# Kernel optimization log

Measured on AMD Instinct MI355X. Metric: run time of the kernel, lower is better.

Reference implementation:

```python
import jax, jax.numpy as jnp
import numpy as np

B = 2; C = 128; HEADS = 4
D, H, W = 16, 56, 56
WD, WH, WW = 8, 7, 7
SD, SH, SW = 4, 3, 3
N = WD * WH * WW  # 392 tokens per window
ND, NH, NW = D // WD, H // WH, W // WW
NWIN = ND * NH * NW  # windows per batch element
EPS = 1e-5

def _rel_index():
    # standard Swin3D relative position index, [N, N]
    coords = np.stack(np.meshgrid(np.arange(WD), np.arange(WH), np.arange(WW), indexing='ij'))
    coords = coords.reshape(3, -1)
    rel = coords[:, :, None] - coords[:, None, :]  # 3,N,N
    rel = rel.transpose(1, 2, 0).astype(np.int64)
    rel[:, :, 0] += WD - 1; rel[:, :, 1] += WH - 1; rel[:, :, 2] += WW - 1
    rel[:, :, 0] *= (2 * WH - 1) * (2 * WW - 1)
    rel[:, :, 1] *= (2 * WW - 1)
    return jnp.asarray(rel.sum(-1))

REL_IDX = _rel_index()

def _attn_mask():
    # region labels for shifted windows; mask = -100 where tokens come from different regions
    img = np.zeros((D, H, W), np.int32)
    cnt = 0
    for d in (slice(0, -WD), slice(-WD, -SD), slice(-SD, None)):
        for h in (slice(0, -WH), slice(-WH, -SH), slice(-SH, None)):
            for w in (slice(0, -WW), slice(-WW, -SW), slice(-SW, None)):
                img[d, h, w] = cnt; cnt += 1
    m = img.reshape(ND, WD, NH, WH, NW, WW).transpose(0, 2, 4, 1, 3, 5).reshape(-1, N)
    am = m[:, None, :] - m[:, :, None]
    return jnp.asarray(np.where(am != 0, -100.0, 0.0).astype(np.float32))  # [NWIN, N, N]

ATTN_MASK = _attn_mask()

def _ln_channel(x, w, b):
    # LayerNorm over channel dim of [B,C,D,H,W]
    mu = x.mean(1, keepdims=True)
    var = x.var(1, keepdims=True)
    xn = (x - mu) * jax.lax.rsqrt(var + EPS)
    return xn * w[None, :, None, None, None] + b[None, :, None, None, None]

def setup_inputs() -> dict:
    key = jax.random.key(0)
    ks = jax.random.split(key, 6)
    s = 0.02
    return {
        'x': jax.random.normal(ks[0], (B, C, D, H, W), jnp.float32),
        'norm1_w': jnp.ones((C,), jnp.float32),
        'norm1_b': jnp.zeros((C,), jnp.float32),
        'qkv_w': jax.random.normal(ks[1], (3 * C, C), jnp.float32) * s,
        'qkv_b': jnp.zeros((3 * C,), jnp.float32),
        'rpb': jax.random.normal(ks[2], ((2 * WD - 1) * (2 * WH - 1) * (2 * WW - 1), HEADS), jnp.float32) * s,
        'proj_w': jax.random.normal(ks[3], (C, C), jnp.float32) * s,
        'proj_b': jnp.zeros((C,), jnp.float32),
        'norm2_w': jnp.ones((C,), jnp.float32),
        'norm2_b': jnp.zeros((C,), jnp.float32),
        'fc1_w': jax.random.normal(ks[4], (4 * C, C), jnp.float32) * s,
        'fc1_b': jnp.zeros((4 * C,), jnp.float32),
        'fc2_w': jax.random.normal(ks[5], (C, 4 * C), jnp.float32) * s,
        'fc2_b': jnp.zeros((C,), jnp.float32),
    }

def reference(x, norm1_w, norm1_b, qkv_w, qkv_b, rpb, proj_w, proj_b,
              norm2_w, norm2_b, fc1_w, fc1_b, fc2_w, fc2_b):
    hd = C // HEADS
    shortcut = x
    h = _ln_channel(x, norm1_w, norm1_b)
    h = jnp.roll(h, (-SD, -SH, -SW), axis=(2, 3, 4))
    # window partition: [B,C,D,H,W] -> [B*NWIN, N, C]
    h = jnp.transpose(h, (0, 2, 3, 4, 1))  # B,D,H,W,C
    win = h.reshape(B, ND, WD, NH, WH, NW, WW, C)
    win = win.transpose(0, 1, 3, 5, 2, 4, 6, 7).reshape(B * NWIN, N, C)
    # windowed multi-head attention
    qkv = win @ qkv_w.T + qkv_b                      # [BW, N, 3C]
    qkv = qkv.reshape(B * NWIN, N, 3, HEADS, hd).transpose(2, 0, 3, 1, 4)
    q, k, v = qkv[0], qkv[1], qkv[2]                 # [BW, heads, N, hd]
    attn = jnp.einsum('whnd,whmd->whnm', q * (hd ** -0.5), k)
    bias = rpb[REL_IDX].transpose(2, 0, 1)           # [heads, N, N]
    attn = attn + bias[None]
    attn = attn.reshape(B, NWIN, HEADS, N, N) + ATTN_MASK[None, :, None]
    attn = jax.nn.softmax(attn, axis=-1).reshape(B * NWIN, HEADS, N, N)
    out = jnp.einsum('whnm,whmd->whnd', attn, v)
    out = out.transpose(0, 2, 1, 3).reshape(B * NWIN, N, C)
    out = out @ proj_w.T + proj_b
    # window reverse: [B*NWIN, N, C] -> [B,C,D,H,W]
    out = out.reshape(B, ND, NH, NW, WD, WH, WW, C)
    out = out.transpose(0, 1, 4, 2, 5, 3, 6, 7).reshape(B, D, H, W, C)
    out = jnp.transpose(out, (0, 4, 1, 2, 3))
    out = jnp.roll(out, (SD, SH, SW), axis=(2, 3, 4))
    x = shortcut + out
    # FFN (pointwise over channels)
    h2 = _ln_channel(x, norm2_w, norm2_b)
    h2 = jnp.einsum('oc,bcdhw->bodhw', fc1_w, h2) + fc1_b[None, :, None, None, None]
    h2 = jax.nn.gelu(h2)
    h2 = jnp.einsum('oc,bcdhw->bodhw', fc2_w, h2) + fc2_b[None, :, None, None, None]
    return x + h2
```

## Files before the change

### kernel.cpp

```cpp
#include <hip/hip_runtime.h>

#define DEV __device__ __forceinline__

using bf16x8 = __attribute__((ext_vector_type(8))) __bf16;
using f32x4  = __attribute__((ext_vector_type(4))) float;

namespace {
constexpr int SPAT = 50176;
constexpr int TOK  = 100352;
constexpr int NTOK = 392;
constexpr int NTP  = 416;
}

DEV float bf2f(short s){ unsigned u = ((unsigned)(unsigned short)s) << 16; float f; __builtin_memcpy(&f, &u, 4); return f; }
DEV short f2bf(float f){ unsigned u; __builtin_memcpy(&u, &f, 4); u = (u + 0x7fffu + ((u >> 16) & 1u)) >> 16; return (short)u; }
DEV f32x4 mfma16(bf16x8 a, bf16x8 b, f32x4 c){ return __builtin_amdgcn_mfma_f32_16x16x32_bf16(a, b, c, 0, 0, 0); }

DEV int swin_label(int wi, int n){
  int nd = (wi >> 6) & 1, nh = (wi >> 3) & 7, nw = wi & 7;
  int wd = n / 49, wh = (n / 7) % 7, ww = n % 7;
  int d = nd * 8 + wd, h = nh * 7 + wh, w = nw * 7 + ww;
  int ld = d < 8 ? 0 : (d < 12 ? 1 : 2);
  int lh = h < 49 ? 0 : (h < 53 ? 1 : 2);
  int lw = w < 49 ? 0 : (w < 53 ? 1 : 2);
  return ld * 9 + lh * 3 + lw;
}

__global__ __launch_bounds__(256) void k_convert(const float* __restrict__ qkvw, const float* __restrict__ projw,
                                                 const float* __restrict__ fc1w, const float* __restrict__ fc2w,
                                                 short* __restrict__ wq, short* __restrict__ wp,
                                                 short* __restrict__ w1, short* __restrict__ w2){
  int i = blockIdx.x * 256 + threadIdx.x;
  if (i < 49152)        wq[i]          = f2bf(qkvw[i]);
  else if (i < 65536)   wp[i - 49152]  = f2bf(projw[i - 49152]);
  else if (i < 131072)  w1[i - 65536]  = f2bf(fc1w[i - 65536]);
  else if (i < 196608)  w2[i - 131072] = f2bf(fc2w[i - 131072]);
}

__global__ __launch_bounds__(256) void k_ln1(const float* __restrict__ x, const float* __restrict__ w,
                                             const float* __restrict__ b, short* __restrict__ win){
  int m = blockIdx.x * 256 + threadIdx.x;
  int bb = m / SPAT, p = m % SPAT;
  const float* xp = x + (size_t)bb * 128 * SPAT + p;
  float s = 0.f, s2 = 0.f;
  for (int c = 0; c < 128; c++){ float v = xp[(size_t)c * SPAT]; s += v; s2 += v * v; }
  float mu = s * (1.f / 128.f);
  float var = s2 * (1.f / 128.f) - mu * mu;
  float rs = rsqrtf(var + 1e-5f);
  int d = p / 3136, hw = p % 3136, h = hw / 56, wq = hw % 56;
  int dr = (d + 12) & 15, hr = (h + 53) % 56, wr = (wq + 53) % 56;
  int nd = dr >> 3, wd = dr & 7, nh = hr / 7, wh = hr % 7, nw = wr / 7, ww = wr % 7;
  int wi = ((bb * 2 + nd) << 6) + (nh << 3) + nw;
  int n = (wd * 7 + wh) * 7 + ww;
  short* dst = win + (size_t)(wi * NTOK + n) * 128;
  for (int c = 0; c < 128; c++){
    float v = (xp[(size_t)c * SPAT] - mu) * rs * w[c] + b[c];
    dst[c] = f2bf(v);
  }
}

__global__ __launch_bounds__(256) void k_bias(const float* __restrict__ rpb, float* __restrict__ bias){
  int t = blockIdx.x * 256 + threadIdx.x;
  if (t >= NTOK * NTOK) return;
  int i = t / NTOK, j = t % NTOK;
  int wdi = i / 49, whi = (i / 7) % 7, wwi = i % 7;
  int wdj = j / 49, whj = (j / 7) % 7, wwj = j % 7;
  int idx = (wdi - wdj + 7) * 169 + (whi - whj + 6) * 13 + (wwi - wwj + 6);
  for (int h = 0; h < 4; h++)
    bias[((size_t)h * NTOK + i) * NTOK + j] = rpb[idx * 4 + h];
}

__global__ __launch_bounds__(256) void k_qkv(const short* __restrict__ win, const short* __restrict__ wq,
                                             const float* __restrict__ qb, short* __restrict__ Q,
                                             short* __restrict__ K, short* __restrict__ Vt){
  int lane = threadIdx.x & 63, wv = threadIdx.x >> 6;
  int m0 = (blockIdx.x % 1568) * 64 + wv * 16;
  int c0 = (blockIdx.x / 1568) * 64;
  int cc = lane & 15, g = lane >> 4;
  f32x4 acc[4] = {};
  bf16x8 af[4];
  for (int k = 0; k < 4; k++)
    af[k] = *reinterpret_cast<const bf16x8*>(win + (size_t)(m0 + cc) * 128 + k * 32 + g * 8);
  for (int k = 0; k < 4; k++){
    for (int ct = 0; ct < 4; ct++){
      bf16x8 bf = *reinterpret_cast<const bf16x8*>(wq + (size_t)(c0 + ct * 16 + cc) * 128 + k * 32 + g * 8);
      acc[ct] = mfma16(af[k], bf, acc[ct]);
    }
  }
  for (int ct = 0; ct < 4; ct++){
    int o = c0 + ct * 16 + cc;
    int sec = o >> 7, oo = o & 127, head = oo >> 5, hd = oo & 31;
    float bv = qb[o];
    for (int r = 0; r < 4; r++){
      int m = m0 + g * 4 + r;
      float v = acc[ct][r] + bv;
      int wi = m / NTOK, n = m % NTOK;
      if (sec == 0){
        v *= 0.17677669529663687f;
        Q[((size_t)(wi * 4 + head) * NTP + n) * 32 + hd] = f2bf(v);
      } else if (sec == 1){
        K[((size_t)(wi * 4 + head) * NTP + n) * 32 + hd] = f2bf(v);
      } else {
        Vt[((size_t)(wi * 4 + head) * 32 + hd) * NTP + n] = f2bf(v);
      }
    }
  }
}

__global__ __launch_bounds__(256) void k_attn(const short* __restrict__ Q, const short* __restrict__ K,
                                              const short* __restrict__ Vt, const float* __restrict__ bias,
                                              short* __restrict__ O){
  __shared__ short plds[4][16][56];
  int lane = threadIdx.x & 63, wv = threadIdx.x >> 6;
  int wg = blockIdx.x * 4 + wv;
  int qt = wg % 25; int t2 = wg / 25; int head = t2 & 3; int wi = t2 >> 2;
  int q0 = qt * 16;
  const short* Qb = Q + (size_t)(wi * 4 + head) * NTP * 32;
  const short* Kb = K + (size_t)(wi * 4 + head) * NTP * 32;
  const short* Vb = Vt + (size_t)(wi * 4 + head) * 32 * NTP;
  const float* Bb = bias + (size_t)head * NTOK * NTOK;
  int cc = lane & 15, g = lane >> 4;
  bf16x8 qf = *reinterpret_cast<const bf16x8*>(Qb + (q0 + cc) * 32 + g * 8);
  int irow[4], lbli[4];
  for (int r = 0; r < 4; r++){
    int i = q0 + g * 4 + r; irow[r] = i;
    lbli[r] = swin_label(wi, i < NTOK ? i : NTOK - 1);
  }
  float mrun[4], lrun[4];
  f32x4 acc0 = {}, acc1 = {};
  for (int r = 0; r < 4; r++){ mrun[r] = -1e30f; lrun[r] = 0.f; }
  for (int jt = 0; jt < 13; jt++){
    int j0 = jt * 32;
    int jg0 = j0 + cc, jg1 = j0 + 16 + cc;
    bf16x8 kf0 = *reinterpret_cast<const bf16x8*>(Kb + jg0 * 32 + g * 8);
    bf16x8 kf1 = *reinterpret_cast<const bf16x8*>(Kb + jg1 * 32 + g * 8);
    f32x4 z = {};
    f32x4 s0 = mfma16(qf, kf0, z);
    f32x4 s1 = mfma16(qf, kf1, z);
    int lblj0 = jg0 < NTOK ? swin_label(wi, jg0) : -1;
    int lblj1 = jg1 < NTOK ? swin_label(wi, jg1) : -1;
    for (int r = 0; r < 4; r++){
      int ii = irow[r] < NTOK ? irow[r] : NTOK - 1;
      float v0 = (jg0 < NTOK) ? s0[r] + Bb[(size_t)ii * NTOK + jg0] + (lblj0 != lbli[r] ? -100.f : 0.f) : -1e30f;
      float v1 = (jg1 < NTOK) ? s1[r] + Bb[(size_t)ii * NTOK + jg1] + (lblj1 != lbli[r] ? -100.f : 0.f) : -1e30f;
      float vm = fmaxf(v0, v1);
      #pragma unroll
      for (int off = 1; off < 16; off <<= 1) vm = fmaxf(vm, __shfl_xor(vm, off));
      float mn = fmaxf(mrun[r], vm);
      float al = __expf(mrun[r] - mn);
      float p0 = __expf(v0 - mn), p1 = __expf(v1 - mn);
      float ps = p0 + p1;
      #pragma unroll
      for (int off = 1; off < 16; off <<= 1) ps += __shfl_xor(ps, off);
      lrun[r] = lrun[r] * al + ps;
      mrun[r] = mn;
      acc0[r] *= al; acc1[r] *= al;
      int rr = g * 4 + r;
      plds[wv][rr][cc]      = f2bf(p0);
      plds[wv][rr][cc + 16] = f2bf(p1);
    }
    asm volatile("s_waitcnt lgkmcnt(0)" ::: "memory");
    bf16x8 pf  = *reinterpret_cast<const bf16x8*>(&plds[wv][cc][g * 8]);
    bf16x8 vf0 = *reinterpret_cast<const bf16x8*>(Vb + cc * NTP + j0 + g * 8);
    bf16x8 vf1 = *reinterpret_cast<const bf16x8*>(Vb + (cc + 16) * NTP + j0 + g * 8);
    acc0 = mfma16(pf, vf0, acc0);
    acc1 = mfma16(pf, vf1, acc1);
  }
  for (int r = 0; r < 4; r++){
    int i = irow[r];
    if (i < NTOK){
      float inv = 1.f / lrun[r];
      size_t o = (size_t)(wi * NTOK + i) * 128 + head * 32;
      O[o + cc]      = f2bf(acc0[r] * inv);
      O[o + 16 + cc] = f2bf(acc1[r] * inv);
    }
  }
}

__global__ __launch_bounds__(256) void k_proj(const short* __restrict__ A, const short* __restrict__ Bw,
                                              const float* __restrict__ pb, short* __restrict__ Cout){
  int lane = threadIdx.x & 63, wv = threadIdx.x >> 6;
  int m0 = (blockIdx.x % 1568) * 64 + wv * 16;
  int c0 = (blockIdx.x / 1568) * 64;
  int cc = lane & 15, g = lane >> 4;
  f32x4 acc[4] = {};
  bf16x8 af[4];
  for (int k = 0; k < 4; k++)
    af[k] = *reinterpret_cast<const bf16x8*>(A + (size_t)(m0 + cc) * 128 + k * 32 + g * 8);
  for (int k = 0; k < 4; k++){
    for (int ct = 0; ct < 4; ct++){
      bf16x8 bf = *reinterpret_cast<const bf16x8*>(Bw + (size_t)(c0 + ct * 16 + cc) * 128 + k * 32 + g * 8);
      acc[ct] = mfma16(af[k], bf, acc[ct]);
    }
  }
  for (int ct = 0; ct < 4; ct++){
    int o = c0 + ct * 16 + cc;
    float bv = pb[o];
    for (int r = 0; r < 4; r++){
      int m = m0 + g * 4 + r;
      Cout[(size_t)m * 128 + o] = f2bf(acc[ct][r] + bv);
    }
  }
}

__global__ __launch_bounds__(256) void k_res1(const float* __restrict__ x, const short* __restrict__ pwin,
                                              const float* __restrict__ w2, const float* __restrict__ b2,
                                              float* __restrict__ out, short* __restrict__ h2n){
  int m = blockIdx.x * 256 + threadIdx.x;
  int bb = m / SPAT, p = m % SPAT;
  int d = p / 3136, hw = p % 3136, h = hw / 56, wq = hw % 56;
  int dr = (d + 12) & 15, hr = (h + 53) % 56, wr = (wq + 53) % 56;
  int nd = dr >> 3, wd = dr & 7, nh = hr / 7, wh = hr % 7, nw = wr / 7, ww = wr % 7;
  int wi = ((bb * 2 + nd) << 6) + (nh << 3) + nw;
  int n = (wd * 7 + wh) * 7 + ww;
  const float* xp = x + (size_t)bb * 128 * SPAT + p;
  const short* pw = pwin + (size_t)(wi * NTOK + n) * 128;
  float s = 0.f, s2 = 0.f;
  for (int c = 0; c < 128; c++){
    float v = xp[(size_t)c * SPAT] + bf2f(pw[c]);
    s += v; s2 += v * v;
  }
  float mu = s * (1.f / 128.f);
  float var = s2 * (1.f / 128.f) - mu * mu;
  float rs = rsqrtf(var + 1e-5f);
  float* op = out + (size_t)bb * 128 * SPAT + p;
  short* hp = h2n + (size_t)m * 128;
  for (int c = 0; c < 128; c++){
    float v = xp[(size_t)c * SPAT] + bf2f(pw[c]);
    op[(size_t)c * SPAT] = v;
    hp[c] = f2bf((v - mu) * rs * w2[c] + b2[c]);
  }
}

__global__ __launch_bounds__(256) void k_ffn(const short* __restrict__ h2n, const short* __restrict__ w1,
                                             const float* __restrict__ b1, const short* __restrict__ w2,
                                             const float* __restrict__ b2, float* __restrict__ out){
  __shared__ short smid[64 * 520];
  __shared__ float sout[64 * 129];
  int lane = threadIdx.x & 63, wv = threadIdx.x >> 6;
  int t0 = blockIdx.x * 64;
  int cc = lane & 15, g = lane >> 4;
  bf16x8 af[4];
  for (int k = 0; k < 4; k++)
    af[k] = *reinterpret_cast<const bf16x8*>(h2n + (size_t)(t0 + wv * 16 + cc) * 128 + k * 32 + g * 8);
  for (int ct = 0; ct < 32; ct++){
    f32x4 acc = {};
    for (int k = 0; k < 4; k++){
      bf16x8 bf = *reinterpret_cast<const bf16x8*>(w1 + (size_t)(ct * 16 + cc) * 128 + k * 32 + g * 8);
      acc = mfma16(af[k], bf, acc);
    }
    int o = ct * 16 + cc;
    float bv = b1[o];
    for (int r = 0; r < 4; r++){
      int lr = wv * 16 + g * 4 + r;
      float v = acc[r] + bv;
      float ge = 0.5f * v * (1.f + tanhf(0.7978845608028654f * (v + 0.044715f * v * v * v)));
      smid[lr * 520 + o] = f2bf(ge);
    }
  }
  __syncthreads();
  f32x4 acc2[8] = {};
  for (int ks = 0; ks < 16; ks++){
    bf16x8 a = *reinterpret_cast<const bf16x8*>(&smid[(wv * 16 + cc) * 520 + ks * 32 + g * 8]);
    for (int ct = 0; ct < 8; ct++){
      bf16x8 bf = *reinterpret_cast<const bf16x8*>(w2 + (size_t)(ct * 16 + cc) * 512 + ks * 32 + g * 8);
      acc2[ct] = mfma16(a, bf, acc2[ct]);
    }
  }
  for (int ct = 0; ct < 8; ct++){
    int o = ct * 16 + cc;
    float bv = b2[o];
    for (int r = 0; r < 4; r++){
      int lr = wv * 16 + g * 4 + r;
      sout[lr * 129 + o] = acc2[ct][r] + bv;
    }
  }
  __syncthreads();
  int bb = t0 / SPAT, p0 = t0 % SPAT;
  int poff = threadIdx.x & 63;
  int obase = threadIdx.x >> 6;
  float* op = out + (size_t)bb * 128 * SPAT + p0 + poff;
  for (int oi = 0; oi < 32; oi++){
    int o = obase + oi * 4;
    op[(size_t)o * SPAT] += sout[poff * 129 + o];
  }
}

extern "C" void kernel_launch(void* const* d_in, const int* in_sizes, int n_in,
                              void* d_out, int out_size, void* d_ws, size_t ws_size,
                              hipStream_t stream){
  const float* x     = (const float*)d_in[0];
  const float* n1w   = (const float*)d_in[1];
  const float* n1b   = (const float*)d_in[2];
  const float* qkvw  = (const float*)d_in[3];
  const float* qkvb  = (const float*)d_in[4];
  const float* rpb   = (const float*)d_in[5];
  const float* projw = (const float*)d_in[6];
  const float* projb = (const float*)d_in[7];
  const float* n2w   = (const float*)d_in[8];
  const float* n2b   = (const float*)d_in[9];
  const float* fc1w  = (const float*)d_in[10];
  const float* fc1b  = (const float*)d_in[11];
  const float* fc2w  = (const float*)d_in[12];
  const float* fc2b  = (const float*)d_in[13];
  float* out = (float*)d_out;

  char* ws = (char*)d_ws;
  size_t off = 0;
  auto alloc = [&](size_t bytes) -> void* {
    void* p = ws + off;
    off += (bytes + 255) & ~(size_t)255;
    return p;
  };
  short* win  = (short*)alloc((size_t)TOK * 128 * 2);
  short* Obuf = (short*)alloc((size_t)TOK * 128 * 2);
  short* pwin = (short*)alloc((size_t)TOK * 128 * 2);
  short* h2n  = (short*)alloc((size_t)TOK * 128 * 2);
  short* Qb   = (short*)alloc((size_t)1024 * NTP * 32 * 2);
  short* Kb   = (short*)alloc((size_t)1024 * NTP * 32 * 2);
  short* Vtb  = (short*)alloc((size_t)1024 * NTP * 32 * 2);
  float* bias = (float*)alloc((size_t)4 * NTOK * NTOK * 4);
  short* wq   = (short*)alloc(49152 * 2);
  short* wp   = (short*)alloc(16384 * 2);
  short* w1   = (short*)alloc(65536 * 2);
  short* w2   = (short*)alloc(65536 * 2);

  k_convert<<<768, 256, 0, stream>>>(qkvw, projw, fc1w, fc2w, wq, wp, w1, w2);
  k_ln1<<<TOK / 256, 256, 0, stream>>>(x, n1w, n1b, win);
  k_bias<<<(NTOK * NTOK + 255) / 256, 256, 0, stream>>>(rpb, bias);
  k_qkv<<<1568 * 6, 256, 0, stream>>>(win, wq, qkvb, Qb, Kb, Vtb);
  k_attn<<<6400, 256, 0, stream>>>(Qb, Kb, Vtb, bias, Obuf);
  k_proj<<<1568 * 2, 256, 0, stream>>>(Obuf, wp, projb, pwin);
  k_res1<<<TOK / 256, 256, 0, stream>>>(x, pwin, n2w, n2b, out, h2n);
  k_ffn<<<TOK / 64, 256, 0, stream>>>(h2n, w1, fc1b, w2, fc2b, out);
}
```

Baseline: 875.1 us.

## Stage LayerNorm tiles through LDS and split FFN into separate fc1/fc2 kernels

k_ln1 and k_res1 now load 64-token by 128-channel tiles with vectorized coalesced reads into shared memory. They compute statistics with four threads per token and emit bf16 rows with 16-byte stores, replacing the earlier strided per-thread channel loops. The fused FFN kernel, which used large LDS (about 100KB per block, limiting occupancy), is split into k_fc1 and k_fc2. k_fc1 writes a bf16 intermediate to a reused workspace buffer, and k_fc2 rounds its output to bf16 before the residual add. GELU uses an exp-based sigmoid form, and the extra global round trip for the 512-wide intermediate and bf16 output rounding are the trade-offs.

```diff
diff --git a/kernel.cpp b/kernel.cpp
--- a/kernel.cpp
+++ b/kernel.cpp
@@ -4,6 +4,7 @@
 
 using bf16x8 = __attribute__((ext_vector_type(8))) __bf16;
 using f32x4  = __attribute__((ext_vector_type(4))) float;
+using short8 = __attribute__((ext_vector_type(8))) short;
 
 namespace {
 constexpr int SPAT = 50176;
@@ -24,6 +25,14 @@
   int lh = h < 49 ? 0 : (h < 53 ? 1 : 2);
   int lw = w < 49 ? 0 : (w < 53 ? 1 : 2);
   return ld * 9 + lh * 3 + lw;
+}
+
+DEV void roll_map(int bb, int p, int& wi, int& n){
+  int d = p / 3136, hw = p % 3136, h = hw / 56, wq = hw % 56;
+  int dr = (d + 12) & 15, hr = (h + 53) % 56, wr = (wq + 53) % 56;
+  int nd = dr >> 3, wd = dr & 7, nh = hr / 7, wh = hr % 7, nw = wr / 7, ww = wr % 7;
+  wi = ((bb * 2 + nd) << 6) + (nh << 3) + nw;
+  n = (wd * 7 + wh) * 7 + ww;
 }
 
 __global__ __launch_bounds__(256) void k_convert(const float* __restrict__ qkvw, const float* __restrict__ projw,
@@ -39,23 +48,42 @@
 
 __global__ __launch_bounds__(256) void k_ln1(const float* __restrict__ x, const float* __restrict__ w,
                                              const float* __restrict__ b, short* __restrict__ win){
-  int m = blockIdx.x * 256 + threadIdx.x;
-  int bb = m / SPAT, p = m % SPAT;
-  const float* xp = x + (size_t)bb * 128 * SPAT + p;
+  __shared__ float xs[128 * 68];
+  __shared__ float wln[128], bln[128];
+  int t = threadIdx.x;
+  int p0g = blockIdx.x * 64;
+  int bb = p0g / SPAT, ps = p0g % SPAT;
+  const float* xb = x + (size_t)bb * 128 * SPAT + ps;
+  int chunk = t & 15, crow = t >> 4;
+  for (int it = 0; it < 8; it++){
+    int c = it * 16 + crow;
+    f32x4 v = *reinterpret_cast<const f32x4*>(xb + (size_t)c * SPAT + chunk * 4);
+    *reinterpret_cast<f32x4*>(&xs[c * 68 + chunk * 4]) = v;
+  }
+  if (t < 128){ wln[t] = w[t]; bln[t] = b[t]; }
+  __syncthreads();
+  int tl = t >> 2, part = t & 3;
   float s = 0.f, s2 = 0.f;
-  for (int c = 0; c < 128; c++){ float v = xp[(size_t)c * SPAT]; s += v; s2 += v * v; }
+  for (int i = 0; i < 32; i++){
+    float v = xs[(part * 32 + i) * 68 + tl];
+    s += v; s2 += v * v;
+  }
+  s  += __shfl_xor(s, 1);  s  += __shfl_xor(s, 2);
+  s2 += __shfl_xor(s2, 1); s2 += __shfl_xor(s2, 2);
   float mu = s * (1.f / 128.f);
   float var = s2 * (1.f / 128.f) - mu * mu;
   float rs = rsqrtf(var + 1e-5f);
-  int d = p / 3136, hw = p % 3136, h = hw / 56, wq = hw % 56;
-  int dr = (d + 12) & 15, hr = (h + 53) % 56, wr = (wq + 53) % 56;
-  int nd = dr >> 3, wd = dr & 7, nh = hr / 7, wh = hr % 7, nw = wr / 7, ww = wr % 7;
-  int wi = ((bb * 2 + nd) << 6) + (nh << 3) + nw;
-  int n = (wd * 7 + wh) * 7 + ww;
-  short* dst = win + (size_t)(wi * NTOK + n) * 128;
-  for (int c = 0; c < 128; c++){
-    float v = (xp[(size_t)c * SPAT] - mu) * rs * w[c] + b[c];
-    dst[c] = f2bf(v);
+  int wi, n; roll_map(bb, ps + tl, wi, n);
+  short* dst = win + (size_t)(wi * NTOK + n) * 128 + part * 32;
+  #pragma unroll
+  for (int k8 = 0; k8 < 4; k8++){
+    short8 o;
+    #pragma unroll
+    for (int j = 0; j < 8; j++){
+      int c = part * 32 + k8 * 8 + j;
+      o[j] = f2bf((xs[c * 68 + tl] - mu) * rs * wln[c] + bln[c]);
+    }
+    *reinterpret_cast<short8*>(dst + k8 * 8) = o;
   }
 }
 
@@ -206,83 +234,127 @@
 __global__ __launch_bounds__(256) void k_res1(const float* __restrict__ x, const short* __restrict__ pwin,
                                               const float* __restrict__ w2, const float* __restrict__ b2,
                                               float* __restrict__ out, short* __restrict__ h2n){
-  int m = blockIdx.x * 256 + threadIdx.x;
-  int bb = m / SPAT, p = m % SPAT;
-  int d = p / 3136, hw = p % 3136, h = hw / 56, wq = hw % 56;
-  int dr = (d + 12) & 15, hr = (h + 53) % 56, wr = (wq + 53) % 56;
-  int nd = dr >> 3, wd = dr & 7, nh = hr / 7, wh = hr % 7, nw = wr / 7, ww = wr % 7;
-  int wi = ((bb * 2 + nd) << 6) + (nh << 3) + nw;
-  int n = (wd * 7 + wh) * 7 + ww;
-  const float* xp = x + (size_t)bb * 128 * SPAT + p;
-  const short* pw = pwin + (size_t)(wi * NTOK + n) * 128;
+  __shared__ float xs[128 * 68];
+  __shared__ float wln[128], bln[128];
+  int t = threadIdx.x;
+  int p0g = blockIdx.x * 64;
+  int bb = p0g / SPAT, ps = p0g % SPAT;
+  const float* xb = x + (size_t)bb * 128 * SPAT + ps;
+  int chunk = t & 15, crow = t >> 4;
+  for (int it = 0; it < 8; it++){
+    int c = it * 16 + crow;
+    f32x4 v = *reinterpret_cast<const f32x4*>(xb + (size_t)c * SPAT + chunk * 4);
+    *reinterpret_cast<f32x4*>(&xs[c * 68 + chunk * 4]) = v;
+  }
+  if (t < 128){ wln[t] = w2[t]; bln[t] = b2[t]; }
+  __syncthreads();
+  for (int it = 0; it < 4; it++){
+    int r = it * 16 + crow;
+    int wi, n; roll_map(bb, ps + r, wi, n);
+    short8 pv = *reinterpret_cast<const short8*>(pwin + (size_t)(wi * NTOK + n) * 128 + chunk * 8);
+    #pragma unroll
+    for (int j = 0; j < 8; j++)
+      xs[(chunk * 8 + j) * 68 + r] += bf2f(pv[j]);
+  }
+  __syncthreads();
+  float* ob = out + (size_t)bb * 128 * SPAT + ps;
+  for (int it = 0; it < 8; it++){
+    int c = it * 16 + crow;
+    f32x4 v = *reinterpret_cast<f32x4*>(&xs[c * 68 + chunk * 4]);
+    *reinterpret_cast<f32x4*>(ob + (size_t)c * SPAT + chunk * 4) = v;
+  }
+  int tl = t >> 2, part = t & 3;
   float s = 0.f, s2 = 0.f;
-  for (int c = 0; c < 128; c++){
-    float v = xp[(size_t)c * SPAT] + bf2f(pw[c]);
+  for (int i = 0; i < 32; i++){
+    float v = xs[(part * 32 + i) * 68 + tl];
     s += v; s2 += v * v;
   }
+  s  += __shfl_xor(s, 1);  s  += __shfl_xor(s, 2);
+  s2 += __shfl_xor(s2, 1); s2 += __shfl_xor(s2, 2);
   float mu = s * (1.f / 128.f);
   float var = s2 * (1.f / 128.f) - mu * mu;
   float rs = rsqrtf(var + 1e-5f);
-  float* op = out + (size_t)bb * 128 * SPAT + p;
-  short* hp = h2n + (size_t)m * 128;
-  for (int c = 0; c < 128; c++){
-    float v = xp[(size_t)c * SPAT] + bf2f(pw[c]);
-    op[(size_t)c * SPAT] = v;
-    hp[c] = f2bf((v - mu) * rs * w2[c] + b2[c]);
-  }
-}
-
-__global__ __launch_bounds__(256) void k_ffn(const short* __restrict__ h2n, const short* __restrict__ w1,
-                                             const float* __restrict__ b1, const short* __restrict__ w2,
+  short* hp = h2n + (size_t)(p0g + tl) * 128 + part * 32;
+  #pragma unroll
+  for (int k8 = 0; k8 < 4; k8++){
+    short8 o;
+    #pragma unroll
+    for (int j = 0; j < 8; j++){
+      int c = part * 32 + k8 * 8 + j;
+      o[j] = f2bf((xs[c * 68 + tl] - mu) * rs * wln[c] + bln[c]);
+    }
+    *reinterpret_cast<short8*>(hp + k8 * 8) = o;
+  }
+}
+
+__global__ __launch_bounds__(256) void k_fc1(const short* __restrict__ h2n, const short* __restrict__ w1,
+                                             const float* __restrict__ b1, short* __restrict__ mid){
+  __shared__ short smid[64 * 136];
+  int t = threadIdx.x, lane = t & 63, wv = t >> 6;
+  int t0 = (blockIdx.x >> 2) * 64, c0 = (blockIdx.x & 3) * 128;
+  int cc = lane & 15, g = lane >> 4;
+  int m0 = t0 + wv * 16;
+  bf16x8 af[4];
+  for (int k = 0; k < 4; k++)
+    af[k] = *reinterpret_cast<const bf16x8*>(h2n + (size_t)(m0 + cc) * 128 + k * 32 + g * 8);
+  f32x4 acc[8] = {};
+  for (int k = 0; k < 4; k++){
+    #pragma unroll
+    for (int ct = 0; ct < 8; ct++){
+      bf16x8 bf = *reinterpret_cast<const bf16x8*>(w1 + (size_t)(c0 + ct * 16 + cc) * 128 + k * 32 + g * 8);
+      acc[ct] = mfma16(af[k], bf, acc[ct]);
+    }
+  }
+  #pragma unroll
+  for (int ct = 0; ct < 8; ct++){
+    float bv = b1[c0 + ct * 16 + cc];
+    for (int r = 0; r < 4; r++){
+      int lr = wv * 16 + g * 4 + r;
+      float v = acc[ct][r] + bv;
+      float e = __expf(1.5957691216057308f * (v + 0.044715f * v * v * v));
+      smid[lr * 136 + ct * 16 + cc] = f2bf(v * e / (e + 1.f));
+    }
+  }
+  __syncthreads();
+  int chunk = t & 15, row = t >> 4;
+  for (int it = 0; it < 4; it++){
+    int r = it * 16 + row;
+    short8 v = *reinterpret_cast<short8*>(&smid[r * 136 + chunk * 8]);
+    *reinterpret_cast<short8*>(mid + (size_t)(t0 + r) * 512 + c0 + chunk * 8) = v;
+  }
+}
+
+__global__ __launch_bounds__(256) void k_fc2(const short* __restrict__ mid, const short* __restrict__ w2,
                                              const float* __restrict__ b2, float* __restrict__ out){
-  __shared__ short smid[64 * 520];
-  __shared__ float sout[64 * 129];
-  int lane = threadIdx.x & 63, wv = threadIdx.x >> 6;
+  __shared__ short so[64 * 130];
+  int t = threadIdx.x, lane = t & 63, wv = t >> 6;
   int t0 = blockIdx.x * 64;
   int cc = lane & 15, g = lane >> 4;
-  bf16x8 af[4];
-  for (int k = 0; k < 4; k++)
-    af[k] = *reinterpret_cast<const bf16x8*>(h2n + (size_t)(t0 + wv * 16 + cc) * 128 + k * 32 + g * 8);
-  for (int ct = 0; ct < 32; ct++){
-    f32x4 acc = {};
-    for (int k = 0; k < 4; k++){
-      bf16x8 bf = *reinterpret_cast<const bf16x8*>(w1 + (size_t)(ct * 16 + cc) * 128 + k * 32 + g * 8);
-      acc = mfma16(af[k], bf, acc);
-    }
-    int o = ct * 16 + cc;
-    float bv = b1[o];
+  int m0 = t0 + wv * 16;
+  f32x4 acc[8] = {};
+  for (int ks = 0; ks < 16; ks++){
+    bf16x8 a = *reinterpret_cast<const bf16x8*>(mid + (size_t)(m0 + cc) * 512 + ks * 32 + g * 8);
+    #pragma unroll
+    for (int ct = 0; ct < 8; ct++){
+      bf16x8 bf = *reinterpret_cast<const bf16x8*>(w2 + (size_t)(ct * 16 + cc) * 512 + ks * 32 + g * 8);
+      acc[ct] = mfma16(a, bf, acc[ct]);
+    }
+  }
+  #pragma unroll
+  for (int ct = 0; ct < 8; ct++){
+    float bv = b2[ct * 16 + cc];
     for (int r = 0; r < 4; r++){
       int lr = wv * 16 + g * 4 + r;
-      float v = acc[r] + bv;
-      float ge = 0.5f * v * (1.f + tanhf(0.7978845608028654f * (v + 0.044715f * v * v * v)));
-      smid[lr * 520 + o] = f2bf(ge);
+      so[lr * 130 + ct * 16 + cc] = f2bf(acc[ct][r] + bv);
     }
   }
   __syncthreads();
-  f32x4 acc2[8] = {};
-  for (int ks = 0; ks < 16; ks++){
-    bf16x8 a = *reinterpret_cast<const bf16x8*>(&smid[(wv * 16 + cc) * 520 + ks * 32 + g * 8]);
-    for (int ct = 0; ct < 8; ct++){
-      bf16x8 bf = *reinterpret_cast<const bf16x8*>(w2 + (size_t)(ct * 16 + cc) * 512 + ks * 32 + g * 8);
-      acc2[ct] = mfma16(a, bf, acc2[ct]);
-    }
-  }
-  for (int ct = 0; ct < 8; ct++){
-    int o = ct * 16 + cc;
-    float bv = b2[o];
-    for (int r = 0; r < 4; r++){
-      int lr = wv * 16 + g * 4 + r;
-      sout[lr * 129 + o] = acc2[ct][r] + bv;
-    }
-  }
-  __syncthreads();
-  int bb = t0 / SPAT, p0 = t0 % SPAT;
-  int poff = threadIdx.x & 63;
-  int obase = threadIdx.x >> 6;
-  float* op = out + (size_t)bb * 128 * SPAT + p0 + poff;
+  int bb = t0 / SPAT, ps = t0 % SPAT;
+  int poff = t & 63, obase = t >> 6;
+  float* op = out + (size_t)bb * 128 * SPAT + ps + poff;
   for (int oi = 0; oi < 32; oi++){
     int o = obase + oi * 4;
-    op[(size_t)o * SPAT] += sout[poff * 129 + o];
+    op[(size_t)o * SPAT] += bf2f(so[poff * 130 + o]);
   }
 }
 
@@ -312,25 +384,27 @@
     off += (bytes + 255) & ~(size_t)255;
     return p;
   };
-  short* win  = (short*)alloc((size_t)TOK * 128 * 2);
-  short* Obuf = (short*)alloc((size_t)TOK * 128 * 2);
   short* pwin = (short*)alloc((size_t)TOK * 128 * 2);
   short* h2n  = (short*)alloc((size_t)TOK * 128 * 2);
-  short* Qb   = (short*)alloc((size_t)1024 * NTP * 32 * 2);
-  short* Kb   = (short*)alloc((size_t)1024 * NTP * 32 * 2);
-  short* Vtb  = (short*)alloc((size_t)1024 * NTP * 32 * 2);
   float* bias = (float*)alloc((size_t)4 * NTOK * NTOK * 4);
   short* wq   = (short*)alloc(49152 * 2);
   short* wp   = (short*)alloc(16384 * 2);
   short* w1   = (short*)alloc(65536 * 2);
   short* w2   = (short*)alloc(65536 * 2);
+  short* win  = (short*)alloc((size_t)TOK * 128 * 2);
+  short* Obuf = (short*)alloc((size_t)TOK * 128 * 2);
+  short* Qb   = (short*)alloc((size_t)1024 * NTP * 32 * 2);
+  short* Kb   = (short*)alloc((size_t)1024 * NTP * 32 * 2);
+  short* Vtb  = (short*)alloc((size_t)1024 * NTP * 32 * 2);
+  short* mid  = win;
 
   k_convert<<<768, 256, 0, stream>>>(qkvw, projw, fc1w, fc2w, wq, wp, w1, w2);
-  k_ln1<<<TOK / 256, 256, 0, stream>>>(x, n1w, n1b, win);
+  k_ln1<<<TOK / 64, 256, 0, stream>>>(x, n1w, n1b, win);
   k_bias<<<(NTOK * NTOK + 255) / 256, 256, 0, stream>>>(rpb, bias);
   k_qkv<<<1568 * 6, 256, 0, stream>>>(win, wq, qkvb, Qb, Kb, Vtb);
   k_attn<<<6400, 256, 0, stream>>>(Qb, Kb, Vtb, bias, Obuf);
   k_proj<<<1568 * 2, 256, 0, stream>>>(Obuf, wp, projb, pwin);
-  k_res1<<<TOK / 256, 256, 0, stream>>>(x, pwin, n2w, n2b, out, h2n);
-  k_ffn<<<TOK / 64, 256, 0, stream>>>(h2n, w1, fc1b, w2, fc2b, out);
-}
+  k_res1<<<TOK / 64, 256, 0, stream>>>(x, pwin, n2w, n2b, out, h2n);
+  k_fc1<<<1568 * 4, 256, 0, stream>>>(h2n, w1, fc1b, mid);
+  k_fc2<<<1568, 256, 0, stream>>>(mid, w2, fc2b, out);
+}
```

After: 717.3 us. -18.0%, faster.
